# Optimization experiments

Measured on AMD Instinct MI355X. Metric: run time of the kernel, lower is better.

Reference implementation:

```python
import jax, jax.numpy as jnp
import numpy as np

B, N, R = 8, 1024, 8192
D_IN, REL_D = 32, 1
NF_P, NF_R, NF_E, D_OUT = 128, 128, 128, 3
PSTEP = 3


def setup_inputs() -> dict:
    key = jax.random.key(0)
    ks = jax.random.split(key, 26)
    state = jax.random.normal(ks[0], (B, N, D_IN), dtype=jnp.float32)
    # Rr/Rs are one-hot selection matrices [B, N, R]: column j selects the
    # receiver/sender particle of relation j.
    recv = jax.random.randint(ks[1], (B, R), 0, N)
    send = jax.random.randint(ks[2], (B, R), 0, N)
    Rr = jnp.transpose(jax.nn.one_hot(recv, N, dtype=jnp.float32), (0, 2, 1))
    Rs = jnp.transpose(jax.nn.one_hot(send, N, dtype=jnp.float32), (0, 2, 1))
    Ra = jax.random.normal(ks[3], (B, R, REL_D), dtype=jnp.float32)

    def lin(k, i, o):
        kw, kb = jax.random.split(k)
        return (0.02 * jax.random.normal(kw, (i, o), dtype=jnp.float32),
                0.02 * jax.random.normal(kb, (o,), dtype=jnp.float32))

    pe_w0, pe_b0 = lin(ks[4], D_IN, NF_P)
    pe_w1, pe_b1 = lin(ks[5], NF_P, NF_E)
    re_w0, re_b0 = lin(ks[6], 2 * D_IN + REL_D, NF_R)
    re_w1, re_b1 = lin(ks[7], NF_R, NF_R)
    re_w2, re_b2 = lin(ks[8], NF_R, NF_R)
    rp_w, rp_b = lin(ks[9], NF_R + 2 * NF_E, NF_E)   # relation_propagator
    pp_w, pp_b = lin(ks[10], 2 * NF_E, NF_E)          # particle_propagator
    pr_w0, pr_b0 = lin(ks[11], NF_E, NF_E)            # particle_predictor
    pr_w1, pr_b1 = lin(ks[12], NF_E, D_OUT)
    return dict(state=state, Rr=Rr, Rs=Rs, Ra=Ra, pstep=PSTEP,
                pe_w0=pe_w0, pe_b0=pe_b0, pe_w1=pe_w1, pe_b1=pe_b1,
                re_w0=re_w0, re_b0=re_b0, re_w1=re_w1, re_b1=re_b1,
                re_w2=re_w2, re_b2=re_b2, rp_w=rp_w, rp_b=rp_b,
                pp_w=pp_w, pp_b=pp_b, pr_w0=pr_w0, pr_b0=pr_b0,
                pr_w1=pr_w1, pr_b1=pr_b1)


def reference(state, Rr, Rs, Ra, pstep,
              pe_w0, pe_b0, pe_w1, pe_b1,
              re_w0, re_b0, re_w1, re_b1, re_w2, re_b2,
              rp_w, rp_b, pp_w, pp_b,
              pr_w0, pr_b0, pr_w1, pr_b1):
    relu = jax.nn.relu
    # gather particle states into relation slots: Rr^T @ state -> [B, R, D]
    state_r = jnp.einsum('bnr,bnd->brd', Rr, state)
    state_s = jnp.einsum('bnr,bnd->brd', Rs, state)
    # particle encoder: Linear-ReLU-Linear-ReLU
    particle_encode = relu(relu(state @ pe_w0 + pe_b0) @ pe_w1 + pe_b1)  # [B,N,NF_E]
    # relation encoder: 3-layer MLP with ReLU after each layer
    rel_in = jnp.concatenate([state_r, state_s, Ra], axis=2)
    h = relu(rel_in @ re_w0 + re_b0)
    h = relu(h @ re_w1 + re_b1)
    relation_encode = relu(h @ re_w2 + re_b2)  # [B,R,NF_R]

    particle_effect = jnp.zeros((B, N, NF_E), dtype=state.dtype)
    for _ in range(pstep):
        effect_r = jnp.einsum('bnr,bne->bre', Rr, particle_effect)  # gather
        effect_s = jnp.einsum('bnr,bne->bre', Rs, particle_effect)
        rel_x = jnp.concatenate([relation_encode, effect_r, effect_s], axis=2)
        relation_effect = relu(rel_x @ rp_w + rp_b)  # [B,R,NF_E]
        # scatter-add relation effects back to receiver particles
        effect_agg = jnp.einsum('bnr,bre->bne', Rr, relation_effect)
        part_x = jnp.concatenate([particle_encode, effect_agg], axis=2)
        # residual particle propagator: relu(linear(x) + prev_effect)
        particle_effect = relu(part_x @ pp_w + pp_b + particle_effect)
    pred = relu(particle_effect @ pr_w0 + pr_b0) @ pr_w1 + pr_b1  # [B,N,D_OUT]
    return pred
```

## Files before the change

kernel.cpp:

```cpp
#include <hip/hip_runtime.h>

#define NB 8
#define NP 1024
#define NR 8192

typedef unsigned short u16;
typedef __attribute__((ext_vector_type(8))) short bf16x8;
typedef __attribute__((ext_vector_type(4))) float f32x4;

#define MFMA __builtin_amdgcn_mfma_f32_16x16x32_bf16

static __device__ __forceinline__ float bf2f(u16 u) {
    union { unsigned int i; float f; } v; v.i = ((unsigned int)u) << 16; return v.f;
}
static __device__ __forceinline__ unsigned int f2bf(float f) {
    union { float fv; unsigned int i; } v; v.fv = f;
    unsigned int r = v.i + 0x7FFFu + ((v.i >> 16) & 1u);
    return r >> 16;
}
static __device__ __forceinline__ unsigned int pack2(float a, float b) {
    return f2bf(a) | (f2bf(b) << 16);
}
static __device__ __forceinline__ void unpk8(uint4 v, float* o) {
    o[0] = bf2f((u16)(v.x & 0xFFFF)); o[1] = bf2f((u16)(v.x >> 16));
    o[2] = bf2f((u16)(v.y & 0xFFFF)); o[3] = bf2f((u16)(v.y >> 16));
    o[4] = bf2f((u16)(v.z & 0xFFFF)); o[5] = bf2f((u16)(v.z >> 16));
    o[6] = bf2f((u16)(v.w & 0xFFFF)); o[7] = bf2f((u16)(v.w >> 16));
}

__global__ __launch_bounds__(256) void k_indices(
    const uint4* __restrict__ Rr4, const uint4* __restrict__ Rs4,
    u16* __restrict__ recv, u16* __restrict__ send, int* __restrict__ counts)
{
    long i = (long)blockIdx.x * 256 + threadIdx.x;
    int c4 = (int)(i & 2047);
    int n  = (int)((i >> 11) & 1023);
    int b  = (int)(i >> 21);
    int base = b * NR + c4 * 4;
    uint4 vr = Rr4[i];
    uint4 vs = Rs4[i];
    int cnt = 0;
    if (vr.x) { recv[base + 0] = (u16)n; ++cnt; }
    if (vr.y) { recv[base + 1] = (u16)n; ++cnt; }
    if (vr.z) { recv[base + 2] = (u16)n; ++cnt; }
    if (vr.w) { recv[base + 3] = (u16)n; ++cnt; }
    if (cnt) atomicAdd(&counts[b * NP + n], cnt);
    if (vs.x) send[base + 0] = (u16)n;
    if (vs.y) send[base + 1] = (u16)n;
    if (vs.z) send[base + 2] = (u16)n;
    if (vs.w) send[base + 3] = (u16)n;
}

__global__ __launch_bounds__(1024) void k_csr(
    const int* __restrict__ counts, const u16* __restrict__ recv,
    int* __restrict__ row_ptr, u16* __restrict__ rel_idx)
{
    __shared__ int s[NP];
    __shared__ int cur[NP];
    int b = blockIdx.x, t = threadIdx.x;
    int v = counts[b * NP + t];
    s[t] = v;
    __syncthreads();
    #pragma unroll
    for (int off = 1; off < NP; off <<= 1) {
        int add = (t >= off) ? s[t - off] : 0;
        __syncthreads();
        s[t] += add;
        __syncthreads();
    }
    int excl = s[t] - v;
    row_ptr[b * (NP + 1) + t] = excl;
    cur[t] = excl;
    if (t == NP - 1) row_ptr[b * (NP + 1) + NP] = s[t];
    __syncthreads();
    #pragma unroll
    for (int k = 0; k < NR / 1024; ++k) {
        int r = k * 1024 + t;
        int p = recv[b * NR + r] & 1023;
        int pos = atomicAdd(&cur[p], 1) & 8191;
        rel_idx[b * NR + pos] = (u16)r;
    }
}

__global__ __launch_bounds__(256) void k_prep(
    const float* __restrict__ w0, const float* __restrict__ w1,
    const float* __restrict__ w2, const float* __restrict__ w3,
    const float* __restrict__ w4, const float* __restrict__ w5,
    const float* __restrict__ w6, const float* __restrict__ w7,
    bf16x8* __restrict__ out, int* __restrict__ counts)
{
    int tid = threadIdx.x;
    {
        int4* c4 = (int4*)(counts + blockIdx.x * NP);
        if (tid < 256) c4[tid] = make_int4(0, 0, 0, 0);
    }
    const float* W; int KC, kv, off;
    switch (blockIdx.x) {
        case 0:  W = w0; KC = 3;  kv = 65;  off = 0;  break;
        case 1:  W = w1; KC = 4;  kv = 128; off = 6;  break;
        case 2:  W = w2; KC = 4;  kv = 128; off = 14; break;
        case 3:  W = w3; KC = 1;  kv = 32;  off = 22; break;
        case 4:  W = w4; KC = 4;  kv = 128; off = 24; break;
        case 5:  W = w5; KC = 12; kv = 384; off = 32; break;
        case 6:  W = w6; KC = 8;  kv = 256; off = 56; break;
        default: W = w7; KC = 4;  kv = 128; off = 72; break;
    }
    int wave = tid >> 6, quad = (tid >> 4) & 3, l16 = tid & 15;
    for (int kc = 0; kc < KC; ++kc)
      for (int nt = 0; nt < 2; ++nt) {
        bf16x8 f;
        #pragma unroll
        for (int j = 0; j < 8; ++j) {
            int k = kc*32 + quad*8 + j;
            f[j] = (k < kv) ? (short)f2bf(W[k*128 + wave*32 + nt*16 + l16]) : (short)0;
        }
        out[(off + kc*2 + nt)*256 + tid] = f;
      }
}

template<int KC>
static __device__ __forceinline__ void load_wfrag(
    const bf16x8* __restrict__ fb, bf16x8 (&wf)[KC][2], int tid)
{
    #pragma unroll
    for (int kc = 0; kc < KC; ++kc)
      #pragma unroll
      for (int nt = 0; nt < 2; ++nt)
        wf[kc][nt] = fb[(kc*2 + nt)*256 + tid];
}

template<int KC, int LDA>
static __device__ __forceinline__ void mfma_compute(
    const u16* xlds, const bf16x8 (&wf)[KC][2], f32x4 (&acc)[4][2],
    int l16, int quad)
{
    #pragma unroll
    for (int kc = 0; kc < KC; ++kc) {
        bf16x8 a[4];
        #pragma unroll
        for (int mt = 0; mt < 4; ++mt)
            a[mt] = *(const bf16x8*)(xlds + (mt*16 + l16)*LDA + kc*32 + quad*8);
        #pragma unroll
        for (int mt = 0; mt < 4; ++mt) {
            acc[mt][0] = MFMA(a[mt], wf[kc][0], acc[mt][0], 0, 0, 0);
            acc[mt][1] = MFMA(a[mt], wf[kc][1], acc[mt][1], 0, 0, 0);
        }
    }
}

static __device__ __forceinline__ void zero_acc(f32x4 (&acc)[4][2]) {
    #pragma unroll
    for (int mt = 0; mt < 4; ++mt)
      #pragma unroll
      for (int nt = 0; nt < 2; ++nt)
        acc[mt][nt] = f32x4{0.f, 0.f, 0.f, 0.f};
}

template<int LDA>
static __device__ __forceinline__ void store_c_lds(
    u16* xlds, const f32x4 (&acc)[4][2], const float* __restrict__ bias,
    int wave, int quad, int l16)
{
    #pragma unroll
    for (int mt = 0; mt < 4; ++mt)
      #pragma unroll
      for (int nt = 0; nt < 2; ++nt) {
        int col = wave*32 + nt*16 + l16;
        float bv = bias[col];
        #pragma unroll
        for (int rg = 0; rg < 4; ++rg)
            xlds[(mt*16 + quad*4 + rg)*LDA + col] =
                (u16)f2bf(fmaxf(acc[mt][nt][rg] + bv, 0.f));
      }
}

template<bool RELU>
static __device__ __forceinline__ void store_c_glob(
    u16* __restrict__ out, long row0, const f32x4 (&acc)[4][2],
    const float* __restrict__ bias, int wave, int quad, int l16)
{
    #pragma unroll
    for (int mt = 0; mt < 4; ++mt)
      #pragma unroll
      for (int nt = 0; nt < 2; ++nt) {
        int col = wave*32 + nt*16 + l16;
        float bv = bias[col];
        #pragma unroll
        for (int rg = 0; rg < 4; ++rg) {
            long r = row0 + mt*16 + quad*4 + rg;
            float v = acc[mt][nt][rg] + bv;
            if (RELU) v = fmaxf(v, 0.f);
            out[r*128 + col] = (u16)f2bf(v);
        }
      }
}

__global__ __launch_bounds__(256) void k_enc4(
    const float* __restrict__ state, const float* __restrict__ Ra,
    const u16* __restrict__ recv, const u16* __restrict__ send,
    const bf16x8* __restrict__ fb0, const float* __restrict__ b0,
    const bf16x8* __restrict__ fb1, const float* __restrict__ b1,
    const bf16x8* __restrict__ fb2, const float* __restrict__ b2,
    const bf16x8* __restrict__ fbP, const float* __restrict__ bP,
    u16* __restrict__ bufP)
{
    constexpr int LDA = 136;
    __shared__ __align__(16) u16 xlds[64 * LDA];
    const int tid = threadIdx.x;
    const int wave = tid >> 6, quad = (tid >> 4) & 3, l16 = tid & 15;
    const int row0 = blockIdx.x * 64;
    const int b = row0 >> 13;

    {
        int r = tid >> 2, tt = tid & 3;
        int rel = row0 + r;
        u16* dst = xlds + r * LDA;
        int ri = recv[rel] & 1023;
        int si = send[rel] & 1023;
        const float* rrow = state + ((long)(b*NP + ri)) * 32;
        const float* srow = state + ((long)(b*NP + si)) * 32;
        float4 a0 = *(const float4*)(rrow + tt*8);
        float4 a1 = *(const float4*)(rrow + tt*8 + 4);
        uint4 o;
        o.x = pack2(a0.x, a0.y); o.y = pack2(a0.z, a0.w);
        o.z = pack2(a1.x, a1.y); o.w = pack2(a1.z, a1.w);
        *(uint4*)(dst + tt*8) = o;
        float4 s0 = *(const float4*)(srow + tt*8);
        float4 s1 = *(const float4*)(srow + tt*8 + 4);
        o.x = pack2(s0.x, s0.y); o.y = pack2(s0.z, s0.w);
        o.z = pack2(s1.x, s1.y); o.w = pack2(s1.z, s1.w);
        *(uint4*)(dst + 32 + tt*8) = o;
        if (tt == 3) {
            uint4 z = make_uint4(0, 0, 0, 0);
            *(uint4*)(dst + 64) = z; *(uint4*)(dst + 72) = z;
            *(uint4*)(dst + 80) = z; *(uint4*)(dst + 88) = z;
            dst[64] = (u16)f2bf(Ra[rel]);
        }
    }
    __syncthreads();

    f32x4 acc[4][2];
    zero_acc(acc);
    {
        bf16x8 wf[3][2];
        load_wfrag<3>(fb0, wf, tid);
        mfma_compute<3, LDA>(xlds, wf, acc, l16, quad);
    }
    __syncthreads();
    store_c_lds<LDA>(xlds, acc, b0, wave, quad, l16);
    __syncthreads();
    zero_acc(acc);
    {
        bf16x8 wf[4][2];
        load_wfrag<4>(fb1, wf, tid);
        mfma_compute<4, LDA>(xlds, wf, acc, l16, quad);
    }
    __syncthreads();
    store_c_lds<LDA>(xlds, acc, b1, wave, quad, l16);
    __syncthreads();
    zero_acc(acc);
    {
        bf16x8 wf[4][2];
        load_wfrag<4>(fb2, wf, tid);
        mfma_compute<4, LDA>(xlds, wf, acc, l16, quad);
    }
    __syncthreads();
    store_c_lds<LDA>(xlds, acc, b2, wave, quad, l16);
    __syncthreads();
    zero_acc(acc);
    {
        bf16x8 wf[4][2];
        load_wfrag<4>(fbP, wf, tid);
        mfma_compute<4, LDA>(xlds, wf, acc, l16, quad);
    }
    store_c_glob<false>(bufP, row0, acc, bP, wave, quad, l16);
}

__global__ __launch_bounds__(256) void k_pe2(
    const float* __restrict__ state,
    const bf16x8* __restrict__ fb0, const float* __restrict__ b0,
    const bf16x8* __restrict__ fb1, const float* __restrict__ b1,
    u16* __restrict__ out)
{
    constexpr int LDA = 136;
    __shared__ __align__(16) u16 xlds[64 * LDA];
    const int tid = threadIdx.x;
    const int wave = tid >> 6, quad = (tid >> 4) & 3, l16 = tid & 15;
    const long row0 = (long)blockIdx.x * 64;

    for (int idx = tid; idx < 64 * 8; idx += 256) {
        int r = idx >> 3, c = idx & 7;
        float4 v = *(const float4*)(state + (row0 + r)*32 + c*4);
        uint2 o; o.x = pack2(v.x, v.y); o.y = pack2(v.z, v.w);
        *(uint2*)(xlds + r*LDA + c*4) = o;
    }
    __syncthreads();

    f32x4 acc[4][2];
    zero_acc(acc);
    {
        bf16x8 wf[1][2];
        load_wfrag<1>(fb0, wf, tid);
        mfma_compute<1, LDA>(xlds, wf, acc, l16, quad);
    }
    __syncthreads();
    store_c_lds<LDA>(xlds, acc, b0, wave, quad, l16);
    __syncthreads();
    zero_acc(acc);
    {
        bf16x8 wf[4][2];
        load_wfrag<4>(fb1, wf, tid);
        mfma_compute<4, LDA>(xlds, wf, acc, l16, quad);
    }
    store_c_glob<true>(out, row0, acc, b1, wave, quad, l16);
}

__global__ __launch_bounds__(256) void k_gemmUV(
    const float* __restrict__ peff32, const bf16x8* __restrict__ fbU,
    const bf16x8* __restrict__ fbV, u16* __restrict__ UV)
{
    constexpr int LDA = 136;
    __shared__ __align__(16) u16 xlds[64 * LDA];
    const int tid = threadIdx.x;
    const int wave = tid >> 6, quad = (tid >> 4) & 3, l16 = tid & 15;
    const long row0 = (long)blockIdx.x * 64;

    for (int idx = tid; idx < 64 * 32; idx += 256) {
        int r = idx >> 5, c = idx & 31;
        float4 v = *(const float4*)(peff32 + (row0 + r)*128 + c*4);
        uint2 o; o.x = pack2(v.x, v.y); o.y = pack2(v.z, v.w);
        *(uint2*)(xlds + r*LDA + c*4) = o;
    }
    __syncthreads();

    #pragma unroll
    for (int half = 0; half < 2; ++half) {
        bf16x8 wf[4][2];
        load_wfrag<4>(half ? fbV : fbU, wf, tid);
        f32x4 acc[4][2];
        zero_acc(acc);
        mfma_compute<4, LDA>(xlds, wf, acc, l16, quad);
        #pragma unroll
        for (int mt = 0; mt < 4; ++mt)
          #pragma unroll
          for (int nt = 0; nt < 2; ++nt) {
            int col = half*128 + wave*32 + nt*16 + l16;
            #pragma unroll
            for (int rg = 0; rg < 4; ++rg) {
                long r = row0 + mt*16 + quad*4 + rg;
                UV[r*256 + col] = (u16)f2bf(acc[mt][nt][rg]);
            }
          }
    }
}

template<bool STEP1>
__global__ __launch_bounds__(256) void k_pp(
    const u16* __restrict__ penc, const u16* __restrict__ bufP,
    const u16* __restrict__ UV, const int* __restrict__ row_ptr,
    const u16* __restrict__ rel_idx, const u16* __restrict__ send,
    const bf16x8* __restrict__ fb, const float* __restrict__ bias,
    float* __restrict__ peff32_io)
{
    constexpr int LDA = 264;
    __shared__ __align__(16) u16 xlds[64 * LDA];
    const int tid = threadIdx.x;
    const int wave = tid >> 6, quad = (tid >> 4) & 3, l16 = tid & 15;
    const long row0 = (long)blockIdx.x * 64;

    for (int idx = tid; idx < 1024; idx += 256) {
        int r = idx >> 4, c = idx & 15;
        *(uint4*)(xlds + r*LDA + c*8) = *(const uint4*)(penc + (row0 + r)*128 + c*8);
    }
    {
        int pp = tid >> 2;
        int cq = tid & 3;
        int gp = (int)row0 + pp;
        int b = gp >> 10, pl = gp & 1023;
        const int* rp = row_ptr + b * (NP + 1);
        int s0 = rp[pl], e0 = rp[pl + 1];
        float a[32];
        #pragma unroll
        for (int t = 0; t < 32; ++t) a[t] = 0.f;
        float uv[32];
        if (!STEP1) {
            const u16* ur = UV + ((long)gp)*256 + cq*32;
            #pragma unroll
            for (int h = 0; h < 4; ++h) unpk8(*(const uint4*)(ur + h*8), uv + h*8);
        }
        for (int j = s0; j < e0; ++j) {
            int rel = rel_idx[b * NR + j] & 8191;
            const u16* prow = bufP + ((long)(b * NR + rel))*128 + cq*32;
            if (STEP1) {
                #pragma unroll
                for (int h = 0; h < 4; ++h) {
                    float pv[8];
                    unpk8(*(const uint4*)(prow + h*8), pv);
                    #pragma unroll
                    for (int e = 0; e < 8; ++e)
                        a[h*8 + e] += fmaxf(pv[e], 0.f);
                }
            } else {
                int sj = send[b * NR + rel] & 1023;
                const u16* vrow = UV + ((long)(b*NP + sj))*256 + 128 + cq*32;
                #pragma unroll
                for (int h = 0; h < 4; ++h) {
                    float pv[8], vv[8];
                    unpk8(*(const uint4*)(prow + h*8), pv);
                    unpk8(*(const uint4*)(vrow + h*8), vv);
                    #pragma unroll
                    for (int e = 0; e < 8; ++e)
                        a[h*8 + e] += fmaxf(pv[e] + uv[h*8 + e] + vv[e], 0.f);
                }
            }
        }
        u16* dst = xlds + pp*LDA + 128 + cq*32;
        #pragma unroll
        for (int h = 0; h < 4; ++h) {
            uint4 o;
            o.x = pack2(a[h*8+0], a[h*8+1]); o.y = pack2(a[h*8+2], a[h*8+3]);
            o.z = pack2(a[h*8+4], a[h*8+5]); o.w = pack2(a[h*8+6], a[h*8+7]);
            *(uint4*)(dst + h*8) = o;
        }
    }
    __syncthreads();

    bf16x8 wf[8][2];
    load_wfrag<8>(fb, wf, tid);
    f32x4 acc[4][2];
    zero_acc(acc);
    mfma_compute<8, LDA>(xlds, wf, acc, l16, quad);

    #pragma unroll
    for (int mt = 0; mt < 4; ++mt)
      #pragma unroll
      for (int nt = 0; nt < 2; ++nt) {
        int col = wave*32 + nt*16 + l16;
        float bv = bias[col];
        #pragma unroll
        for (int rg = 0; rg < 4; ++rg) {
            long r = row0 + mt*16 + quad*4 + rg;
            float prev = STEP1 ? 0.f : peff32_io[r*128 + col];
            float v = fmaxf(acc[mt][nt][rg] + bv + prev, 0.f);
            peff32_io[r*128 + col] = v;
        }
      }
}

__global__ __launch_bounds__(256) void k_predf(
    const float* __restrict__ peff32, const bf16x8* __restrict__ fb,
    const float* __restrict__ b0, const float* __restrict__ W1,
    const float* __restrict__ b1, float* __restrict__ out)
{
    constexpr int LDA = 136;
    __shared__ __align__(16) u16 xlds[64 * LDA];
    const int tid = threadIdx.x;
    const int wave = tid >> 6, quad = (tid >> 4) & 3, l16 = tid & 15;
    const long row0 = (long)blockIdx.x * 64;

    bf16x8 wf[4][2];
    load_wfrag<4>(fb, wf, tid);

    for (int idx = tid; idx < 64 * 32; idx += 256) {
        int r = idx >> 5, c = idx & 31;
        float4 v = *(const float4*)(peff32 + (row0 + r)*128 + c*4);
        uint2 o; o.x = pack2(v.x, v.y); o.y = pack2(v.z, v.w);
        *(uint2*)(xlds + r*LDA + c*4) = o;
    }
    __syncthreads();

    f32x4 acc[4][2];
    zero_acc(acc);
    mfma_compute<4, LDA>(xlds, wf, acc, l16, quad);
    __syncthreads();
    store_c_lds<LDA>(xlds, acc, b0, wave, quad, l16);
    __syncthreads();

    if (tid < 192) {
        int row = tid / 3, col = tid - row * 3;
        float s = b1[col];
        const u16* hr = xlds + row * LDA;
        #pragma unroll 8
        for (int k = 0; k < 128; ++k) s += bf2f(hr[k]) * W1[k*3 + col];
        out[(row0 + row)*3 + col] = s;
    }
}

extern "C" void kernel_launch(void* const* d_in, const int* in_sizes, int n_in,
                              void* d_out, int out_size, void* d_ws, size_t ws_size,
                              hipStream_t stream) {
    const float* state = (const float*)d_in[0];
    const float* Rr    = (const float*)d_in[1];
    const float* Rs    = (const float*)d_in[2];
    const float* Ra    = (const float*)d_in[3];
    const float* pe_w0 = (const float*)d_in[5];
    const float* pe_b0 = (const float*)d_in[6];
    const float* pe_w1 = (const float*)d_in[7];
    const float* pe_b1 = (const float*)d_in[8];
    const float* re_w0 = (const float*)d_in[9];
    const float* re_b0 = (const float*)d_in[10];
    const float* re_w1 = (const float*)d_in[11];
    const float* re_b1 = (const float*)d_in[12];
    const float* re_w2 = (const float*)d_in[13];
    const float* re_b2 = (const float*)d_in[14];
    const float* rp_w  = (const float*)d_in[15];
    const float* rp_b  = (const float*)d_in[16];
    const float* pp_w  = (const float*)d_in[17];
    const float* pp_b  = (const float*)d_in[18];
    const float* pr_w0 = (const float*)d_in[19];
    const float* pr_b0 = (const float*)d_in[20];
    const float* pr_w1 = (const float*)d_in[21];
    const float* pr_b1 = (const float*)d_in[22];

    char* p = (char*)d_ws;
    u16*    bufP    = (u16*)p;    p += (size_t)NB*NR*128*2;
    u16*    UV      = (u16*)p;    p += (size_t)NB*NP*256*2;
    float*  peff32  = (float*)p;  p += (size_t)NB*NP*128*4;
    u16*    penc    = (u16*)p;    p += (size_t)NB*NP*128*2;
    bf16x8* wfrag   = (bf16x8*)p; p += (size_t)80*256*16;
    int*    counts  = (int*)p;    p += (size_t)NB*NP*4;
    int*    row_ptr = (int*)p;    p += (size_t)NB*(NP+1)*4 + 12;
    u16*    recv    = (u16*)p;    p += (size_t)NB*NR*2;
    u16*    send    = (u16*)p;    p += (size_t)NB*NR*2;
    u16*    rel_idx = (u16*)p;    p += (size_t)NB*NR*2;

    const bf16x8* f_re0 = wfrag + 0*256;
    const bf16x8* f_re1 = wfrag + 6*256;
    const bf16x8* f_re2 = wfrag + 14*256;
    const bf16x8* f_pe0 = wfrag + 22*256;
    const bf16x8* f_pe1 = wfrag + 24*256;
    const bf16x8* f_rpP = wfrag + 32*256;
    const bf16x8* f_rpU = wfrag + 40*256;
    const bf16x8* f_rpV = wfrag + 48*256;
    const bf16x8* f_pp  = wfrag + 56*256;
    const bf16x8* f_pr0 = wfrag + 72*256;

    k_prep<<<8, 256, 0, stream>>>(re_w0, re_w1, re_w2, pe_w0, pe_w1, rp_w, pp_w, pr_w0,
                                  wfrag, counts);
    k_indices<<<65536, 256, 0, stream>>>((const uint4*)Rr, (const uint4*)Rs, recv, send, counts);
    k_csr<<<NB, 1024, 0, stream>>>(counts, recv, row_ptr, rel_idx);
    k_enc4<<<1024, 256, 0, stream>>>(state, Ra, recv, send,
                                     f_re0, re_b0, f_re1, re_b1, f_re2, re_b2,
                                     f_rpP, rp_b, bufP);
    k_pe2<<<128, 256, 0, stream>>>(state, f_pe0, pe_b0, f_pe1, pe_b1, penc);
    k_pp<true><<<128, 256, 0, stream>>>(penc, bufP, UV, row_ptr, rel_idx, send,
                                        f_pp, pp_b, peff32);
    for (int s = 1; s < 3; ++s) {
        k_gemmUV<<<128, 256, 0, stream>>>(peff32, f_rpU, f_rpV, UV);
        k_pp<false><<<128, 256, 0, stream>>>(penc, bufP, UV, row_ptr, rel_idx, send,
                                             f_pp, pp_b, peff32);
    }
    k_predf<<<128, 256, 0, stream>>>(peff32, f_pr0, pr_b0, pr_w1, pr_b1, (float*)d_out);
}
```

Baseline: 723.4 us.

## Fuse UV GEMM and predictor into propagation kernel, merge encoders, in-block CSR counts

Computes the per-particle receiver counts inside the CSR kernel with shared-memory atomics, which drops the global counts buffer, its zeroing and the global atomics in the index pass. The relation and particle encoders are merged into one launch. The UV projection and the final predictor move into the propagation kernel, with ping-pong UV buffers, and that kernel now uses 32-row tiles so it launches more blocks. The aim is fewer launches and fewer fp32 round trips through global memory, at the cost of more work per propagation block and smaller MFMA tiles.

Measured after the change: 674.3 us. 6.8% less time.

```diff
diff --git a/kernel.cpp b/kernel.cpp
--- a/kernel.cpp
+++ b/kernel.cpp
@@ -30,7 +30,7 @@
 
 __global__ __launch_bounds__(256) void k_indices(
     const uint4* __restrict__ Rr4, const uint4* __restrict__ Rs4,
-    u16* __restrict__ recv, u16* __restrict__ send, int* __restrict__ counts)
+    u16* __restrict__ recv, u16* __restrict__ send)
 {
     long i = (long)blockIdx.x * 256 + threadIdx.x;
     int c4 = (int)(i & 2047);
@@ -39,12 +39,10 @@
     int base = b * NR + c4 * 4;
     uint4 vr = Rr4[i];
     uint4 vs = Rs4[i];
-    int cnt = 0;
-    if (vr.x) { recv[base + 0] = (u16)n; ++cnt; }
-    if (vr.y) { recv[base + 1] = (u16)n; ++cnt; }
-    if (vr.z) { recv[base + 2] = (u16)n; ++cnt; }
-    if (vr.w) { recv[base + 3] = (u16)n; ++cnt; }
-    if (cnt) atomicAdd(&counts[b * NP + n], cnt);
+    if (vr.x) recv[base + 0] = (u16)n;
+    if (vr.y) recv[base + 1] = (u16)n;
+    if (vr.z) recv[base + 2] = (u16)n;
+    if (vr.w) recv[base + 3] = (u16)n;
     if (vs.x) send[base + 0] = (u16)n;
     if (vs.y) send[base + 1] = (u16)n;
     if (vs.z) send[base + 2] = (u16)n;
@@ -52,13 +50,22 @@
 }
 
 __global__ __launch_bounds__(1024) void k_csr(
-    const int* __restrict__ counts, const u16* __restrict__ recv,
-    int* __restrict__ row_ptr, u16* __restrict__ rel_idx)
+    const u16* __restrict__ recv, int* __restrict__ row_ptr,
+    u16* __restrict__ rel_idx)
 {
     __shared__ int s[NP];
     __shared__ int cur[NP];
     int b = blockIdx.x, t = threadIdx.x;
-    int v = counts[b * NP + t];
+    cur[t] = 0;
+    __syncthreads();
+    int pv[NR / 1024];
+    #pragma unroll
+    for (int k = 0; k < NR / 1024; ++k) {
+        pv[k] = recv[b * NR + k * 1024 + t] & 1023;
+        atomicAdd(&cur[pv[k]], 1);
+    }
+    __syncthreads();
+    int v = cur[t];
     s[t] = v;
     __syncthreads();
     #pragma unroll
@@ -75,10 +82,8 @@
     __syncthreads();
     #pragma unroll
     for (int k = 0; k < NR / 1024; ++k) {
-        int r = k * 1024 + t;
-        int p = recv[b * NR + r] & 1023;
-        int pos = atomicAdd(&cur[p], 1) & 8191;
-        rel_idx[b * NR + pos] = (u16)r;
+        int pos = atomicAdd(&cur[pv[k]], 1) & 8191;
+        rel_idx[b * NR + pos] = (u16)(k * 1024 + t);
     }
 }
 
@@ -87,13 +92,8 @@
     const float* __restrict__ w2, const float* __restrict__ w3,
     const float* __restrict__ w4, const float* __restrict__ w5,
     const float* __restrict__ w6, const float* __restrict__ w7,
-    bf16x8* __restrict__ out, int* __restrict__ counts)
-{
-    int tid = threadIdx.x;
-    {
-        int4* c4 = (int4*)(counts + blockIdx.x * NP);
-        if (tid < 256) c4[tid] = make_int4(0, 0, 0, 0);
-    }
+    bf16x8* __restrict__ out)
+{
     const float* W; int KC, kv, off;
     switch (blockIdx.x) {
         case 0:  W = w0; KC = 3;  kv = 65;  off = 0;  break;
@@ -105,6 +105,7 @@
         case 6:  W = w6; KC = 8;  kv = 256; off = 56; break;
         default: W = w7; KC = 4;  kv = 128; off = 72; break;
     }
+    int tid = threadIdx.x;
     int wave = tid >> 6, quad = (tid >> 4) & 3, l16 = tid & 15;
     for (int kc = 0; kc < KC; ++kc)
       for (int nt = 0; nt < 2; ++nt) {
@@ -129,58 +130,59 @@
         wf[kc][nt] = fb[(kc*2 + nt)*256 + tid];
 }
 
-template<int KC, int LDA>
+template<int MT, int KC, int LDA>
 static __device__ __forceinline__ void mfma_compute(
-    const u16* xlds, const bf16x8 (&wf)[KC][2], f32x4 (&acc)[4][2],
+    const u16* xlds, const bf16x8 (&wf)[KC][2], f32x4 (&acc)[MT][2],
     int l16, int quad)
 {
     #pragma unroll
     for (int kc = 0; kc < KC; ++kc) {
-        bf16x8 a[4];
-        #pragma unroll
-        for (int mt = 0; mt < 4; ++mt)
+        bf16x8 a[MT];
+        #pragma unroll
+        for (int mt = 0; mt < MT; ++mt)
             a[mt] = *(const bf16x8*)(xlds + (mt*16 + l16)*LDA + kc*32 + quad*8);
         #pragma unroll
-        for (int mt = 0; mt < 4; ++mt) {
+        for (int mt = 0; mt < MT; ++mt) {
             acc[mt][0] = MFMA(a[mt], wf[kc][0], acc[mt][0], 0, 0, 0);
             acc[mt][1] = MFMA(a[mt], wf[kc][1], acc[mt][1], 0, 0, 0);
         }
     }
 }
 
-static __device__ __forceinline__ void zero_acc(f32x4 (&acc)[4][2]) {
-    #pragma unroll
-    for (int mt = 0; mt < 4; ++mt)
+template<int MT>
+static __device__ __forceinline__ void zero_acc(f32x4 (&acc)[MT][2]) {
+    #pragma unroll
+    for (int mt = 0; mt < MT; ++mt)
       #pragma unroll
       for (int nt = 0; nt < 2; ++nt)
         acc[mt][nt] = f32x4{0.f, 0.f, 0.f, 0.f};
 }
 
-template<int LDA>
+template<int MT, int LDA>
 static __device__ __forceinline__ void store_c_lds(
-    u16* xlds, const f32x4 (&acc)[4][2], const float* __restrict__ bias,
-    int wave, int quad, int l16)
-{
-    #pragma unroll
-    for (int mt = 0; mt < 4; ++mt)
+    u16* xlds, const f32x4 (&acc)[MT][2], const float* __restrict__ bias,
+    int wave, int quad, int l16, int coloff = 0)
+{
+    #pragma unroll
+    for (int mt = 0; mt < MT; ++mt)
       #pragma unroll
       for (int nt = 0; nt < 2; ++nt) {
         int col = wave*32 + nt*16 + l16;
         float bv = bias[col];
         #pragma unroll
         for (int rg = 0; rg < 4; ++rg)
-            xlds[(mt*16 + quad*4 + rg)*LDA + col] =
+            xlds[(mt*16 + quad*4 + rg)*LDA + coloff + col] =
                 (u16)f2bf(fmaxf(acc[mt][nt][rg] + bv, 0.f));
       }
 }
 
-template<bool RELU>
+template<int MT, bool RELU>
 static __device__ __forceinline__ void store_c_glob(
-    u16* __restrict__ out, long row0, const f32x4 (&acc)[4][2],
+    u16* __restrict__ out, long row0, const f32x4 (&acc)[MT][2],
     const float* __restrict__ bias, int wave, int quad, int l16)
 {
     #pragma unroll
-    for (int mt = 0; mt < 4; ++mt)
+    for (int mt = 0; mt < MT; ++mt)
       #pragma unroll
       for (int nt = 0; nt < 2; ++nt) {
         int col = wave*32 + nt*16 + l16;
@@ -195,294 +197,247 @@
       }
 }
 
-__global__ __launch_bounds__(256) void k_enc4(
+__global__ __launch_bounds__(256) void k_encpe(
     const float* __restrict__ state, const float* __restrict__ Ra,
     const u16* __restrict__ recv, const u16* __restrict__ send,
-    const bf16x8* __restrict__ fb0, const float* __restrict__ b0,
-    const bf16x8* __restrict__ fb1, const float* __restrict__ b1,
-    const bf16x8* __restrict__ fb2, const float* __restrict__ b2,
-    const bf16x8* __restrict__ fbP, const float* __restrict__ bP,
-    u16* __restrict__ bufP)
+    const bf16x8* __restrict__ f_re0, const float* __restrict__ re_b0,
+    const bf16x8* __restrict__ f_re1, const float* __restrict__ re_b1,
+    const bf16x8* __restrict__ f_re2, const float* __restrict__ re_b2,
+    const bf16x8* __restrict__ f_rpP, const float* __restrict__ rp_b,
+    u16* __restrict__ bufP,
+    const bf16x8* __restrict__ f_pe0, const float* __restrict__ pe_b0,
+    const bf16x8* __restrict__ f_pe1, const float* __restrict__ pe_b1,
+    u16* __restrict__ penc)
 {
     constexpr int LDA = 136;
     __shared__ __align__(16) u16 xlds[64 * LDA];
     const int tid = threadIdx.x;
     const int wave = tid >> 6, quad = (tid >> 4) & 3, l16 = tid & 15;
-    const int row0 = blockIdx.x * 64;
-    const int b = row0 >> 13;
-
-    {
-        int r = tid >> 2, tt = tid & 3;
-        int rel = row0 + r;
-        u16* dst = xlds + r * LDA;
-        int ri = recv[rel] & 1023;
-        int si = send[rel] & 1023;
-        const float* rrow = state + ((long)(b*NP + ri)) * 32;
-        const float* srow = state + ((long)(b*NP + si)) * 32;
-        float4 a0 = *(const float4*)(rrow + tt*8);
-        float4 a1 = *(const float4*)(rrow + tt*8 + 4);
-        uint4 o;
-        o.x = pack2(a0.x, a0.y); o.y = pack2(a0.z, a0.w);
-        o.z = pack2(a1.x, a1.y); o.w = pack2(a1.z, a1.w);
-        *(uint4*)(dst + tt*8) = o;
-        float4 s0 = *(const float4*)(srow + tt*8);
-        float4 s1 = *(const float4*)(srow + tt*8 + 4);
-        o.x = pack2(s0.x, s0.y); o.y = pack2(s0.z, s0.w);
-        o.z = pack2(s1.x, s1.y); o.w = pack2(s1.z, s1.w);
-        *(uint4*)(dst + 32 + tt*8) = o;
-        if (tt == 3) {
-            uint4 z = make_uint4(0, 0, 0, 0);
-            *(uint4*)(dst + 64) = z; *(uint4*)(dst + 72) = z;
-            *(uint4*)(dst + 80) = z; *(uint4*)(dst + 88) = z;
-            dst[64] = (u16)f2bf(Ra[rel]);
-        }
-    }
-    __syncthreads();
-
     f32x4 acc[4][2];
-    zero_acc(acc);
-    {
-        bf16x8 wf[3][2];
-        load_wfrag<3>(fb0, wf, tid);
-        mfma_compute<3, LDA>(xlds, wf, acc, l16, quad);
-    }
-    __syncthreads();
-    store_c_lds<LDA>(xlds, acc, b0, wave, quad, l16);
-    __syncthreads();
-    zero_acc(acc);
-    {
-        bf16x8 wf[4][2];
-        load_wfrag<4>(fb1, wf, tid);
-        mfma_compute<4, LDA>(xlds, wf, acc, l16, quad);
-    }
-    __syncthreads();
-    store_c_lds<LDA>(xlds, acc, b1, wave, quad, l16);
-    __syncthreads();
-    zero_acc(acc);
-    {
-        bf16x8 wf[4][2];
-        load_wfrag<4>(fb2, wf, tid);
-        mfma_compute<4, LDA>(xlds, wf, acc, l16, quad);
-    }
-    __syncthreads();
-    store_c_lds<LDA>(xlds, acc, b2, wave, quad, l16);
-    __syncthreads();
-    zero_acc(acc);
-    {
-        bf16x8 wf[4][2];
-        load_wfrag<4>(fbP, wf, tid);
-        mfma_compute<4, LDA>(xlds, wf, acc, l16, quad);
-    }
-    store_c_glob<false>(bufP, row0, acc, bP, wave, quad, l16);
-}
-
-__global__ __launch_bounds__(256) void k_pe2(
-    const float* __restrict__ state,
-    const bf16x8* __restrict__ fb0, const float* __restrict__ b0,
-    const bf16x8* __restrict__ fb1, const float* __restrict__ b1,
-    u16* __restrict__ out)
-{
-    constexpr int LDA = 136;
-    __shared__ __align__(16) u16 xlds[64 * LDA];
+
+    if (blockIdx.x < 1024) {
+        const int row0 = blockIdx.x * 64;
+        const int b = row0 >> 13;
+        {
+            int r = tid >> 2, tt = tid & 3;
+            int rel = row0 + r;
+            u16* dst = xlds + r * LDA;
+            int ri = recv[rel] & 1023;
+            int si = send[rel] & 1023;
+            const float* rrow = state + ((long)(b*NP + ri)) * 32;
+            const float* srow = state + ((long)(b*NP + si)) * 32;
+            float4 a0 = *(const float4*)(rrow + tt*8);
+            float4 a1 = *(const float4*)(rrow + tt*8 + 4);
+            uint4 o;
+            o.x = pack2(a0.x, a0.y); o.y = pack2(a0.z, a0.w);
+            o.z = pack2(a1.x, a1.y); o.w = pack2(a1.z, a1.w);
+            *(uint4*)(dst + tt*8) = o;
+            float4 s0 = *(const float4*)(srow + tt*8);
+            float4 s1 = *(const float4*)(srow + tt*8 + 4);
+            o.x = pack2(s0.x, s0.y); o.y = pack2(s0.z, s0.w);
+            o.z = pack2(s1.x, s1.y); o.w = pack2(s1.z, s1.w);
+            *(uint4*)(dst + 32 + tt*8) = o;
+            if (tt == 3) {
+                uint4 z = make_uint4(0, 0, 0, 0);
+                *(uint4*)(dst + 64) = z; *(uint4*)(dst + 72) = z;
+                *(uint4*)(dst + 80) = z; *(uint4*)(dst + 88) = z;
+                dst[64] = (u16)f2bf(Ra[rel]);
+            }
+        }
+        __syncthreads();
+        zero_acc<4>(acc);
+        {
+            bf16x8 wf[3][2];
+            load_wfrag<3>(f_re0, wf, tid);
+            mfma_compute<4, 3, LDA>(xlds, wf, acc, l16, quad);
+        }
+        __syncthreads();
+        store_c_lds<4, LDA>(xlds, acc, re_b0, wave, quad, l16);
+        __syncthreads();
+        zero_acc<4>(acc);
+        {
+            bf16x8 wf[4][2];
+            load_wfrag<4>(f_re1, wf, tid);
+            mfma_compute<4, 4, LDA>(xlds, wf, acc, l16, quad);
+        }
+        __syncthreads();
+        store_c_lds<4, LDA>(xlds, acc, re_b1, wave, quad, l16);
+        __syncthreads();
+        zero_acc<4>(acc);
+        {
+            bf16x8 wf[4][2];
+            load_wfrag<4>(f_re2, wf, tid);
+            mfma_compute<4, 4, LDA>(xlds, wf, acc, l16, quad);
+        }
+        __syncthreads();
+        store_c_lds<4, LDA>(xlds, acc, re_b2, wave, quad, l16);
+        __syncthreads();
+        zero_acc<4>(acc);
+        {
+            bf16x8 wf[4][2];
+            load_wfrag<4>(f_rpP, wf, tid);
+            mfma_compute<4, 4, LDA>(xlds, wf, acc, l16, quad);
+        }
+        store_c_glob<4, false>(bufP, row0, acc, rp_b, wave, quad, l16);
+    } else {
+        const long row0 = (long)(blockIdx.x - 1024) * 64;
+        for (int idx = tid; idx < 64 * 8; idx += 256) {
+            int r = idx >> 3, c = idx & 7;
+            float4 v = *(const float4*)(state + (row0 + r)*32 + c*4);
+            uint2 o; o.x = pack2(v.x, v.y); o.y = pack2(v.z, v.w);
+            *(uint2*)(xlds + r*LDA + c*4) = o;
+        }
+        __syncthreads();
+        zero_acc<4>(acc);
+        {
+            bf16x8 wf[1][2];
+            load_wfrag<1>(f_pe0, wf, tid);
+            mfma_compute<4, 1, LDA>(xlds, wf, acc, l16, quad);
+        }
+        __syncthreads();
+        store_c_lds<4, LDA>(xlds, acc, pe_b0, wave, quad, l16);
+        __syncthreads();
+        zero_acc<4>(acc);
+        {
+            bf16x8 wf[4][2];
+            load_wfrag<4>(f_pe1, wf, tid);
+            mfma_compute<4, 4, LDA>(xlds, wf, acc, l16, quad);
+        }
+        store_c_glob<4, true>(penc, row0, acc, pe_b1, wave, quad, l16);
+    }
+}
+
+template<bool STEP1, bool MAKEUV, bool LAST>
+__global__ __launch_bounds__(256) void k_pp(
+    const u16* __restrict__ penc, const u16* __restrict__ bufP,
+    const u16* __restrict__ UV_in, u16* __restrict__ UV_out,
+    const int* __restrict__ row_ptr, const u16* __restrict__ rel_idx,
+    const u16* __restrict__ send,
+    const bf16x8* __restrict__ f_pp, const float* __restrict__ pp_b,
+    const bf16x8* __restrict__ f_U, const bf16x8* __restrict__ f_V,
+    const bf16x8* __restrict__ f_pr0, const float* __restrict__ pr_b0,
+    const float* __restrict__ pr_w1, const float* __restrict__ pr_b1,
+    float* __restrict__ peff32_io, float* __restrict__ out)
+{
+    constexpr int LDA = 264;
+    __shared__ __align__(16) u16 xlds[32 * LDA];
     const int tid = threadIdx.x;
     const int wave = tid >> 6, quad = (tid >> 4) & 3, l16 = tid & 15;
-    const long row0 = (long)blockIdx.x * 64;
-
-    for (int idx = tid; idx < 64 * 8; idx += 256) {
-        int r = idx >> 3, c = idx & 7;
-        float4 v = *(const float4*)(state + (row0 + r)*32 + c*4);
-        uint2 o; o.x = pack2(v.x, v.y); o.y = pack2(v.z, v.w);
-        *(uint2*)(xlds + r*LDA + c*4) = o;
-    }
-    __syncthreads();
-
-    f32x4 acc[4][2];
-    zero_acc(acc);
-    {
-        bf16x8 wf[1][2];
-        load_wfrag<1>(fb0, wf, tid);
-        mfma_compute<1, LDA>(xlds, wf, acc, l16, quad);
-    }
-    __syncthreads();
-    store_c_lds<LDA>(xlds, acc, b0, wave, quad, l16);
-    __syncthreads();
-    zero_acc(acc);
-    {
-        bf16x8 wf[4][2];
-        load_wfrag<4>(fb1, wf, tid);
-        mfma_compute<4, LDA>(xlds, wf, acc, l16, quad);
-    }
-    store_c_glob<true>(out, row0, acc, b1, wave, quad, l16);
-}
-
-__global__ __launch_bounds__(256) void k_gemmUV(
-    const float* __restrict__ peff32, const bf16x8* __restrict__ fbU,
-    const bf16x8* __restrict__ fbV, u16* __restrict__ UV)
-{
-    constexpr int LDA = 136;
-    __shared__ __align__(16) u16 xlds[64 * LDA];
-    const int tid = threadIdx.x;
-    const int wave = tid >> 6, quad = (tid >> 4) & 3, l16 = tid & 15;
-    const long row0 = (long)blockIdx.x * 64;
-
-    for (int idx = tid; idx < 64 * 32; idx += 256) {
-        int r = idx >> 5, c = idx & 31;
-        float4 v = *(const float4*)(peff32 + (row0 + r)*128 + c*4);
-        uint2 o; o.x = pack2(v.x, v.y); o.y = pack2(v.z, v.w);
-        *(uint2*)(xlds + r*LDA + c*4) = o;
-    }
-    __syncthreads();
-
-    #pragma unroll
-    for (int half = 0; half < 2; ++half) {
-        bf16x8 wf[4][2];
-        load_wfrag<4>(half ? fbV : fbU, wf, tid);
-        f32x4 acc[4][2];
-        zero_acc(acc);
-        mfma_compute<4, LDA>(xlds, wf, acc, l16, quad);
-        #pragma unroll
-        for (int mt = 0; mt < 4; ++mt)
-          #pragma unroll
-          for (int nt = 0; nt < 2; ++nt) {
-            int col = half*128 + wave*32 + nt*16 + l16;
-            #pragma unroll
-            for (int rg = 0; rg < 4; ++rg) {
-                long r = row0 + mt*16 + quad*4 + rg;
-                UV[r*256 + col] = (u16)f2bf(acc[mt][nt][rg]);
-            }
-          }
-    }
-}
-
-template<bool STEP1>
-__global__ __launch_bounds__(256) void k_pp(
-    const u16* __restrict__ penc, const u16* __restrict__ bufP,
-    const u16* __restrict__ UV, const int* __restrict__ row_ptr,
-    const u16* __restrict__ rel_idx, const u16* __restrict__ send,
-    const bf16x8* __restrict__ fb, const float* __restrict__ bias,
-    float* __restrict__ peff32_io)
-{
-    constexpr int LDA = 264;
-    __shared__ __align__(16) u16 xlds[64 * LDA];
-    const int tid = threadIdx.x;
-    const int wave = tid >> 6, quad = (tid >> 4) & 3, l16 = tid & 15;
-    const long row0 = (long)blockIdx.x * 64;
-
-    for (int idx = tid; idx < 1024; idx += 256) {
+    const long row0 = (long)blockIdx.x * 32;
+
+    for (int idx = tid; idx < 512; idx += 256) {
         int r = idx >> 4, c = idx & 15;
         *(uint4*)(xlds + r*LDA + c*8) = *(const uint4*)(penc + (row0 + r)*128 + c*8);
     }
     {
-        int pp = tid >> 2;
-        int cq = tid & 3;
+        int pp = tid >> 3;
+        int cq = tid & 7;
         int gp = (int)row0 + pp;
         int b = gp >> 10, pl = gp & 1023;
         const int* rp = row_ptr + b * (NP + 1);
         int s0 = rp[pl], e0 = rp[pl + 1];
-        float a[32];
-        #pragma unroll
-        for (int t = 0; t < 32; ++t) a[t] = 0.f;
-        float uv[32];
+        float a[16];
+        #pragma unroll
+        for (int t = 0; t < 16; ++t) a[t] = 0.f;
+        float uv[16];
         if (!STEP1) {
-            const u16* ur = UV + ((long)gp)*256 + cq*32;
-            #pragma unroll
-            for (int h = 0; h < 4; ++h) unpk8(*(const uint4*)(ur + h*8), uv + h*8);
+            const u16* ur = UV_in + ((long)gp)*256 + cq*16;
+            unpk8(*(const uint4*)ur, uv);
+            unpk8(*(const uint4*)(ur + 8), uv + 8);
         }
         for (int j = s0; j < e0; ++j) {
             int rel = rel_idx[b * NR + j] & 8191;
-            const u16* prow = bufP + ((long)(b * NR + rel))*128 + cq*32;
+            const u16* prow = bufP + ((long)(b * NR + rel))*128 + cq*16;
+            float pv[16];
+            unpk8(*(const uint4*)prow, pv);
+            unpk8(*(const uint4*)(prow + 8), pv + 8);
             if (STEP1) {
                 #pragma unroll
-                for (int h = 0; h < 4; ++h) {
-                    float pv[8];
-                    unpk8(*(const uint4*)(prow + h*8), pv);
-                    #pragma unroll
-                    for (int e = 0; e < 8; ++e)
-                        a[h*8 + e] += fmaxf(pv[e], 0.f);
-                }
+                for (int e = 0; e < 16; ++e) a[e] += fmaxf(pv[e], 0.f);
             } else {
                 int sj = send[b * NR + rel] & 1023;
-                const u16* vrow = UV + ((long)(b*NP + sj))*256 + 128 + cq*32;
+                const u16* vrow = UV_in + ((long)(b*NP + sj))*256 + 128 + cq*16;
+                float vv[16];
+                unpk8(*(const uint4*)vrow, vv);
+                unpk8(*(const uint4*)(vrow + 8), vv + 8);
                 #pragma unroll
-                for (int h = 0; h < 4; ++h) {
-                    float pv[8], vv[8];
-                    unpk8(*(const uint4*)(prow + h*8), pv);
-                    unpk8(*(const uint4*)(vrow + h*8), vv);
-                    #pragma unroll
-                    for (int e = 0; e < 8; ++e)
-                        a[h*8 + e] += fmaxf(pv[e] + uv[h*8 + e] + vv[e], 0.f);
-                }
+                for (int e = 0; e < 16; ++e)
+                    a[e] += fmaxf(pv[e] + uv[e] + vv[e], 0.f);
             }
         }
-        u16* dst = xlds + pp*LDA + 128 + cq*32;
-        #pragma unroll
-        for (int h = 0; h < 4; ++h) {
-            uint4 o;
-            o.x = pack2(a[h*8+0], a[h*8+1]); o.y = pack2(a[h*8+2], a[h*8+3]);
-            o.z = pack2(a[h*8+4], a[h*8+5]); o.w = pack2(a[h*8+6], a[h*8+7]);
-            *(uint4*)(dst + h*8) = o;
-        }
-    }
-    __syncthreads();
-
-    bf16x8 wf[8][2];
-    load_wfrag<8>(fb, wf, tid);
-    f32x4 acc[4][2];
-    zero_acc(acc);
-    mfma_compute<8, LDA>(xlds, wf, acc, l16, quad);
-
-    #pragma unroll
-    for (int mt = 0; mt < 4; ++mt)
+        u16* dst = xlds + pp*LDA + 128 + cq*16;
+        uint4 o;
+        o.x = pack2(a[0], a[1]);   o.y = pack2(a[2], a[3]);
+        o.z = pack2(a[4], a[5]);   o.w = pack2(a[6], a[7]);
+        *(uint4*)dst = o;
+        o.x = pack2(a[8], a[9]);   o.y = pack2(a[10], a[11]);
+        o.z = pack2(a[12], a[13]); o.w = pack2(a[14], a[15]);
+        *(uint4*)(dst + 8) = o;
+    }
+    __syncthreads();
+
+    f32x4 acc[2][2];
+    {
+        bf16x8 wf[8][2];
+        load_wfrag<8>(f_pp, wf, tid);
+        zero_acc<2>(acc);
+        mfma_compute<2, 8, LDA>(xlds, wf, acc, l16, quad);
+    }
+    __syncthreads();
+
+    #pragma unroll
+    for (int mt = 0; mt < 2; ++mt)
       #pragma unroll
       for (int nt = 0; nt < 2; ++nt) {
         int col = wave*32 + nt*16 + l16;
-        float bv = bias[col];
+        float bv = pp_b[col];
         #pragma unroll
         for (int rg = 0; rg < 4; ++rg) {
-            long r = row0 + mt*16 + quad*4 + rg;
+            int rloc = mt*16 + quad*4 + rg;
+            long r = row0 + rloc;
             float prev = STEP1 ? 0.f : peff32_io[r*128 + col];
             float v = fmaxf(acc[mt][nt][rg] + bv + prev, 0.f);
-            peff32_io[r*128 + col] = v;
+            if (!LAST) peff32_io[r*128 + col] = v;
+            xlds[rloc*LDA + col] = (u16)f2bf(v);
         }
       }
-}
-
-__global__ __launch_bounds__(256) void k_predf(
-    const float* __restrict__ peff32, const bf16x8* __restrict__ fb,
-    const float* __restrict__ b0, const float* __restrict__ W1,
-    const float* __restrict__ b1, float* __restrict__ out)
-{
-    constexpr int LDA = 136;
-    __shared__ __align__(16) u16 xlds[64 * LDA];
-    const int tid = threadIdx.x;
-    const int wave = tid >> 6, quad = (tid >> 4) & 3, l16 = tid & 15;
-    const long row0 = (long)blockIdx.x * 64;
-
-    bf16x8 wf[4][2];
-    load_wfrag<4>(fb, wf, tid);
-
-    for (int idx = tid; idx < 64 * 32; idx += 256) {
-        int r = idx >> 5, c = idx & 31;
-        float4 v = *(const float4*)(peff32 + (row0 + r)*128 + c*4);
-        uint2 o; o.x = pack2(v.x, v.y); o.y = pack2(v.z, v.w);
-        *(uint2*)(xlds + r*LDA + c*4) = o;
-    }
-    __syncthreads();
-
-    f32x4 acc[4][2];
-    zero_acc(acc);
-    mfma_compute<4, LDA>(xlds, wf, acc, l16, quad);
-    __syncthreads();
-    store_c_lds<LDA>(xlds, acc, b0, wave, quad, l16);
-    __syncthreads();
-
-    if (tid < 192) {
-        int row = tid / 3, col = tid - row * 3;
-        float s = b1[col];
-        const u16* hr = xlds + row * LDA;
-        #pragma unroll 8
-        for (int k = 0; k < 128; ++k) s += bf2f(hr[k]) * W1[k*3 + col];
-        out[(row0 + row)*3 + col] = s;
+    __syncthreads();
+
+    if (MAKEUV) {
+        #pragma unroll
+        for (int half = 0; half < 2; ++half) {
+            bf16x8 wf[4][2];
+            load_wfrag<4>(half ? f_V : f_U, wf, tid);
+            zero_acc<2>(acc);
+            mfma_compute<2, 4, LDA>(xlds, wf, acc, l16, quad);
+            #pragma unroll
+            for (int mt = 0; mt < 2; ++mt)
+              #pragma unroll
+              for (int nt = 0; nt < 2; ++nt) {
+                int col = half*128 + wave*32 + nt*16 + l16;
+                #pragma unroll
+                for (int rg = 0; rg < 4; ++rg) {
+                    long r = row0 + mt*16 + quad*4 + rg;
+                    UV_out[r*256 + col] = (u16)f2bf(acc[mt][nt][rg]);
+                }
+              }
+        }
+    }
+    if (LAST) {
+        bf16x8 wf[4][2];
+        load_wfrag<4>(f_pr0, wf, tid);
+        zero_acc<2>(acc);
+        mfma_compute<2, 4, LDA>(xlds, wf, acc, l16, quad);
+        store_c_lds<2, LDA>(xlds, acc, pr_b0, wave, quad, l16, 128);
+        __syncthreads();
+        if (tid < 96) {
+            int row = tid / 3, col = tid - row * 3;
+            float s = pr_b1[col];
+            const u16* hr = xlds + row * LDA + 128;
+            #pragma unroll 8
+            for (int k = 0; k < 128; ++k) s += bf2f(hr[k]) * pr_w1[k*3 + col];
+            out[(row0 + row)*3 + col] = s;
+        }
     }
 }
 
@@ -514,11 +469,11 @@
 
     char* p = (char*)d_ws;
     u16*    bufP    = (u16*)p;    p += (size_t)NB*NR*128*2;
-    u16*    UV      = (u16*)p;    p += (size_t)NB*NP*256*2;
+    u16*    UVa     = (u16*)p;    p += (size_t)NB*NP*256*2;
+    u16*    UVb     = (u16*)p;    p += (size_t)NB*NP*256*2;
     float*  peff32  = (float*)p;  p += (size_t)NB*NP*128*4;
     u16*    penc    = (u16*)p;    p += (size_t)NB*NP*128*2;
     bf16x8* wfrag   = (bf16x8*)p; p += (size_t)80*256*16;
-    int*    counts  = (int*)p;    p += (size_t)NB*NP*4;
     int*    row_ptr = (int*)p;    p += (size_t)NB*(NP+1)*4 + 12;
     u16*    recv    = (u16*)p;    p += (size_t)NB*NR*2;
     u16*    send    = (u16*)p;    p += (size_t)NB*NR*2;
@@ -535,20 +490,22 @@
     const bf16x8* f_pp  = wfrag + 56*256;
     const bf16x8* f_pr0 = wfrag + 72*256;
 
-    k_prep<<<8, 256, 0, stream>>>(re_w0, re_w1, re_w2, pe_w0, pe_w1, rp_w, pp_w, pr_w0,
-                                  wfrag, counts);
-    k_indices<<<65536, 256, 0, stream>>>((const uint4*)Rr, (const uint4*)Rs, recv, send, counts);
-    k_csr<<<NB, 1024, 0, stream>>>(counts, recv, row_ptr, rel_idx);
-    k_enc4<<<1024, 256, 0, stream>>>(state, Ra, recv, send,
-                                     f_re0, re_b0, f_re1, re_b1, f_re2, re_b2,
-                                     f_rpP, rp_b, bufP);
-    k_pe2<<<128, 256, 0, stream>>>(state, f_pe0, pe_b0, f_pe1, pe_b1, penc);
-    k_pp<true><<<128, 256, 0, stream>>>(penc, bufP, UV, row_ptr, rel_idx, send,
-                                        f_pp, pp_b, peff32);
-    for (int s = 1; s < 3; ++s) {
-        k_gemmUV<<<128, 256, 0, stream>>>(peff32, f_rpU, f_rpV, UV);
-        k_pp<false><<<128, 256, 0, stream>>>(penc, bufP, UV, row_ptr, rel_idx, send,
-                                             f_pp, pp_b, peff32);
-    }
-    k_predf<<<128, 256, 0, stream>>>(peff32, f_pr0, pr_b0, pr_w1, pr_b1, (float*)d_out);
-}
+    float* outp = (float*)d_out;
+
+    k_prep<<<8, 256, 0, stream>>>(re_w0, re_w1, re_w2, pe_w0, pe_w1, rp_w, pp_w, pr_w0, wfrag);
+    k_indices<<<65536, 256, 0, stream>>>((const uint4*)Rr, (const uint4*)Rs, recv, send);
+    k_csr<<<NB, 1024, 0, stream>>>(recv, row_ptr, rel_idx);
+    k_encpe<<<1152, 256, 0, stream>>>(state, Ra, recv, send,
+                                      f_re0, re_b0, f_re1, re_b1, f_re2, re_b2,
+                                      f_rpP, rp_b, bufP,
+                                      f_pe0, pe_b0, f_pe1, pe_b1, penc);
+    k_pp<true,  true,  false><<<256, 256, 0, stream>>>(
+        penc, bufP, UVa, UVa, row_ptr, rel_idx, send, f_pp, pp_b,
+        f_rpU, f_rpV, f_pr0, pr_b0, pr_w1, pr_b1, peff32, outp);
+    k_pp<false, true,  false><<<256, 256, 0, stream>>>(
+        penc, bufP, UVa, UVb, row_ptr, rel_idx, send, f_pp, pp_b,
+        f_rpU, f_rpV, f_pr0, pr_b0, pr_w1, pr_b1, peff32, outp);
+    k_pp<false, false, true><<<256, 256, 0, stream>>>(
+        penc, bufP, UVb, UVa, row_ptr, rel_idx, send, f_pp, pp_b,
+        f_rpU, f_rpV, f_pr0, pr_b0, pr_w1, pr_b1, peff32, outp);
+}
```
